# Kernel tuning notes

Hardware: AMD Instinct MI355X
Metric: run time of the kernel (lower is better)

## Reference

```python
import jax, jax.numpy as jnp
import numpy as np

HBLK = 16  # hadamard / nvfp4 block size
FP4_LEVELS = jnp.array([0.0, 0.5, 1.0, 1.5, 2.0, 3.0, 4.0, 6.0], dtype=jnp.float32)
FP4_MIDS = jnp.array([0.25, 0.75, 1.25, 1.75, 2.5, 3.5, 5.0], dtype=jnp.float32)


def _hadamard(n):
    H = np.array([[1.0]])
    while H.shape[0] < n:
        H = np.block([[H, H], [H, -H]])
    return jnp.asarray(H / np.sqrt(n), dtype=jnp.float32)  # orthonormal

H16 = _hadamard(HBLK)


def rht_forward(x, signs):
    # x: [M, K], K % 16 == 0 (no padding needed). Random sign diag then block Hadamard.
    M, K = x.shape
    xb = x.reshape(M, K // HBLK, HBLK)
    return ((xb * signs) @ H16).reshape(M, K)


def q_emulate(x):
    # NVFP4 quantize->dequantize along last dim: blocks of 16, E4M3 block scale = amax/6,
    # round-to-nearest onto E2M1 grid {0,.5,1,1.5,2,3,4,6} (signed).
    M, K = x.shape
    xb = x.reshape(M, K // HBLK, HBLK)
    amax = jnp.max(jnp.abs(xb), axis=-1, keepdims=True)
    scale = (amax / 6.0).astype(jnp.float8_e4m3fn).astype(x.dtype)
    safe = jnp.where(scale == 0, 1.0, scale)
    a = jnp.clip(jnp.abs(xb) / safe, 0.0, 6.0)
    q = FP4_LEVELS[jnp.searchsorted(FP4_MIDS, a)]
    return (jnp.sign(xb) * q * scale).reshape(M, K)


def setup_inputs() -> dict:
    key = jax.random.key(0)
    kx, kw, kb, ks1, ks2 = jax.random.split(key, 5)
    IN, OUT = 4096, 4096
    x = jax.random.normal(kx, (4, 2048, IN), dtype=jnp.float32)
    weight = jax.random.normal(kw, (OUT, IN), dtype=jnp.float32) / np.sqrt(IN)
    bound = 1.0 / np.sqrt(IN)
    bias = jax.random.uniform(kb, (OUT,), dtype=jnp.float32, minval=-bound, maxval=bound)
    signs_in = jnp.where(jax.random.bernoulli(ks1, 0.5, (HBLK,)), 1.0, -1.0).astype(jnp.float32)
    signs_grad = jnp.where(jax.random.bernoulli(ks2, 0.5, (HBLK,)), 1.0, -1.0).astype(jnp.float32)
    return {"x": x, "weight": weight, "bias": bias, "signs_in": signs_in, "signs_grad": signs_grad}


def reference(x, weight, bias, signs_in, signs_grad):
    # signs_grad only used in backward (kept for interface parity).
    x_flat = x.reshape(-1, x.shape[-1])
    x_q = q_emulate(rht_forward(x_flat, signs_in))
    w_q = q_emulate(rht_forward(weight, signs_in))
    y = x_q @ w_q.T + bias
    return y.reshape(*x.shape[:-1], weight.shape[0])
```

## Files before the change

### kernel.cpp

```cpp
#include <hip/hip_runtime.h>
#include <stdint.h>


typedef __bf16 bf16x8 __attribute__((ext_vector_type(8)));
typedef float f32x4 __attribute__((ext_vector_type(4)));


__device__ __forceinline__ float e4m3_rt(float x) {
    unsigned int u = __float_as_uint(x);
    int ex = (int)((u >> 23) & 0xffu) - 127;
    if (ex < -6) ex = -6;
    float qs = __uint_as_float((unsigned)(127 + 3 - ex) << 23);
    float qi = __uint_as_float((unsigned)(127 + ex - 3) << 23);
    return rintf(x * qs) * qi;
}

__global__ __launch_bounds__(256) void quant_rht_kernel(
    const float* __restrict__ X, const float* __restrict__ signs,
    uint16_t* __restrict__ Q, int ngroups)
{
    (void)ngroups;
    __shared__ uint4 sbuf[1024];
    const int t = threadIdx.x;
    const size_t gbase = (size_t)blockIdx.x * 256;

    const uint4* src = (const uint4*)(X + gbase * 16);
#pragma unroll
    for (int it = 0; it < 4; ++it) {
        int c = it * 256 + t;
        sbuf[c ^ ((c >> 3) & 7)] = src[c];
    }
    __syncthreads();

    float tv[16];
#pragma unroll
    for (int i = 0; i < 4; ++i) {
        int c = 4 * t + i;
        uint4 u = sbuf[c ^ ((c >> 3) & 7)];
        tv[4 * i + 0] = __uint_as_float(u.x);
        tv[4 * i + 1] = __uint_as_float(u.y);
        tv[4 * i + 2] = __uint_as_float(u.z);
        tv[4 * i + 3] = __uint_as_float(u.w);
    }

#pragma unroll
    for (int i = 0; i < 16; i++) tv[i] *= signs[i];

#pragma unroll
    for (int len = 1; len < 16; len <<= 1) {
#pragma unroll
        for (int i = 0; i < 16; i += 2 * len) {
#pragma unroll
            for (int j = 0; j < len; j++) {
                float a = tv[i + j], b = tv[i + j + len];
                tv[i + j] = a + b;
                tv[i + j + len] = a - b;
            }
        }
    }
    float amax = 0.0f;
#pragma unroll
    for (int i = 0; i < 16; i++) { tv[i] *= 0.25f; amax = fmaxf(amax, fabsf(tv[i])); }

    float scale = e4m3_rt(amax / 6.0f);
    float safe = (scale == 0.0f) ? 1.0f : scale;

    unsigned int w[8];
#pragma unroll
    for (int i = 0; i < 8; i++) {
        float d01[2];
#pragma unroll
        for (int h = 0; h < 2; h++) {
            float x = tv[2 * i + h];
            float aa = fminf(fabsf(x) / safe, 6.0f);
            float q = aa > 2.5f ? (aa > 5.0f ? 6.0f : (aa > 3.5f ? 4.0f : 3.0f))
                                : (aa > 1.25f ? (aa > 1.75f ? 2.0f : 1.5f)
                                              : (aa > 0.75f ? 1.0f
                                                 : (aa > 0.25f ? 0.5f : 0.0f)));
            d01[h] = copysignf(q * scale, x);
        }
        w[i] = (__float_as_uint(d01[0]) >> 16) |
               (__float_as_uint(d01[1]) & 0xFFFF0000u);
    }

    __syncthreads();
    {
        int c0 = 2 * t, c1 = 2 * t + 1;
        sbuf[c0 ^ ((c0 >> 3) & 7)] = make_uint4(w[0], w[1], w[2], w[3]);
        sbuf[c1 ^ ((c1 >> 3) & 7)] = make_uint4(w[4], w[5], w[6], w[7]);
    }
    __syncthreads();

    uint4* dst = (uint4*)(Q + gbase * 16);
#pragma unroll
    for (int it = 0; it < 2; ++it) {
        int c = it * 256 + t;
        dst[c] = sbuf[c ^ ((c >> 3) & 7)];
    }
}


#define BM 256
#define BN 256

__global__ __launch_bounds__(512, 2) void gemm_bt_bias(
    const uint16_t* __restrict__ A,
    const uint16_t* __restrict__ B,
    const float* __restrict__ bias,
    float* __restrict__ C,
    int M, int N, int K)
{
    __shared__ uint4 sh[8][1024];

    const int tid  = threadIdx.x;
    const int lane = tid & 63;
    const int wave = tid >> 6;
    const int wm = wave >> 2, wn = wave & 3;
    const int lm = lane & 15, g4 = lane >> 4;
    const int bn = blockIdx.x, bm = blockIdx.y;

    const int NT  = K >> 6;
    const int NHT = NT << 2;

    const int p0 = tid, p1 = 512 + tid;
    const int c0 = p0 ^ ((p0 >> 3) & 7);
    const int c1 = p1 ^ ((p1 >> 3) & 7);
    const uint16_t* asrc0 = A + (size_t)(bm * BM + (c0 >> 2)) * K + (c0 & 3) * 8;
    const uint16_t* asrc1 = A + (size_t)(bm * BM + (c1 >> 2)) * K + (c1 & 3) * 8;
    const uint16_t* bsrc0 = B + (size_t)(bn * BN + (c0 >> 2)) * K + (c0 & 3) * 8;
    const uint16_t* bsrc1 = B + (size_t)(bn * BN + (c1 >> 2)) * K + (c1 & 3) * 8;
    char* ldsd0 = (char*)&sh[0][0] + p0 * 16;
    char* ldsd1 = (char*)&sh[0][0] + p1 * 16;

    int aPos[8], bPos[4];
#pragma unroll
    for (int f = 0; f < 8; ++f) {
        int c = (wm * 128 + f * 16 + lm) * 4 + g4;
        aPos[f] = c ^ ((c >> 3) & 7);
    }
#pragma unroll
    for (int f = 0; f < 4; ++f) {
        int c = (wn * 64 + f * 16 + lm) * 4 + g4;
        bPos[f] = c ^ ((c >> 3) & 7);
    }

    f32x4 acc[8][4];
#pragma unroll
    for (int i = 0; i < 8; ++i)
#pragma unroll
        for (int j = 0; j < 4; ++j) acc[i][j] = (f32x4){0.f, 0.f, 0.f, 0.f};
    bf16x8 bfr[4];

#define STAGE(jj) do {                                                        \
    int _j = (jj);                                                            \
    int _koff = (_j < NHT) ? (((_j >> 2) << 6) | (((_j >> 1) & 1) << 5)) : 0; \
    int _sb = (_j & 7) << 14;                                                 \
    const uint16_t* _s0 = (_j & 1) ? bsrc0 : asrc0;                           \
    const uint16_t* _s1 = (_j & 1) ? bsrc1 : asrc1;                           \
    __builtin_amdgcn_global_load_lds(                                         \
        (const __attribute__((address_space(1))) unsigned int*)(_s0 + _koff), \
        (__attribute__((address_space(3))) unsigned int*)(ldsd0 + _sb),       \
        16, 0, 0);                                                            \
    __builtin_amdgcn_global_load_lds(                                         \
        (const __attribute__((address_space(1))) unsigned int*)(_s1 + _koff), \
        (__attribute__((address_space(3))) unsigned int*)(ldsd1 + _sb),       \
        16, 0, 0);                                                            \
} while (0)

#define PHASE(PAR, KS, RH, Q, GATE) do {                                      \
    bf16x8 af_[4];                                                            \
    _Pragma("unroll")                                                         \
    for (int _i = 0; _i < 4; ++_i)                                            \
        af_[_i] = __builtin_bit_cast(bf16x8,                                  \
            sh[4*(PAR) + 2*(KS)][aPos[4*(RH) + _i]]);                         \
    if ((Q) & 1) {                                                            \
        _Pragma("unroll")                                                     \
        for (int _jj = 0; _jj < 4; ++_jj)                                     \
            bfr[_jj] = __builtin_bit_cast(bf16x8,                             \
                sh[4*(PAR) + 2*(KS) + 1][bPos[_jj]]);                         \
    }                                                                         \
    STAGE(hb + 5 + (Q));                                                      \
    __builtin_amdgcn_s_barrier();                                             \
    asm volatile("s_waitcnt lgkmcnt(0)" ::: "memory");                        \
    __builtin_amdgcn_s_setprio(1);                                            \
    _Pragma("unroll")                                                         \
    for (int _i = 0; _i < 4; ++_i)                                            \
        _Pragma("unroll")                                                     \
        for (int _jj = 0; _jj < 4; ++_jj)                                     \
            acc[4*(RH) + _i][_jj] = __builtin_amdgcn_mfma_f32_16x16x32_bf16(  \
                af_[_i], bfr[_jj], acc[4*(RH) + _i][_jj], 0, 0, 0);           \
    __builtin_amdgcn_s_setprio(0);                                            \
    if (GATE) asm volatile("s_waitcnt vmcnt(4)" ::: "memory");                \
    __builtin_amdgcn_s_barrier();                                             \
} while (0)

    STAGE(0); STAGE(1); STAGE(2); STAGE(3); STAGE(4); STAGE(5);
    asm volatile("s_waitcnt vmcnt(4)" ::: "memory");
    __builtin_amdgcn_s_barrier();

    const int NT2 = NT >> 1;
    for (int it2 = 0; it2 < NT2; ++it2) {
        const int hb = it2 << 3;
        PHASE(0, 0, 0, 1, 0);
        PHASE(0, 0, 1, 2, 0);
        PHASE(0, 1, 0, 3, 0);
        PHASE(0, 1, 1, 4, 1);
        PHASE(1, 0, 0, 5, 0);
        PHASE(1, 0, 1, 6, 0);
        PHASE(1, 1, 0, 7, 0);
        PHASE(1, 1, 1, 8, 1);
    }
    asm volatile("s_waitcnt vmcnt(0)" ::: "memory");

#undef PHASE
#undef STAGE

#pragma unroll
    for (int j = 0; j < 4; ++j) {
        int col = bn * BN + wn * 64 + j * 16 + lm;
        float bj = bias[col];
#pragma unroll
        for (int i = 0; i < 8; ++i) {
            int row0 = bm * BM + wm * 128 + i * 16 + g4 * 4;
#pragma unroll
            for (int r = 0; r < 4; ++r) {
                C[(size_t)(row0 + r) * (size_t)N + col] = acc[i][j][r] + bj;
            }
        }
    }
}


extern "C" void kernel_launch(void* const* d_in, const int* in_sizes, int n_in,
                              void* d_out, int out_size, void* d_ws, size_t ws_size,
                              hipStream_t stream)
{
    const float* x        = (const float*)d_in[0];
    const float* w        = (const float*)d_in[1];
    const float* bias     = (const float*)d_in[2];
    const float* signs_in = (const float*)d_in[3];

    const int OUT = in_sizes[2];
    const int IN  = in_sizes[1] / OUT;
    const int M   = in_sizes[0] / IN;

    uint16_t* xq = (uint16_t*)d_ws;
    uint16_t* wq = xq + (size_t)M * (size_t)IN;
    (void)ws_size; (void)n_in; (void)out_size;

    int ngx = (int)((size_t)M * IN / 16);
    int ngw = (int)((size_t)OUT * IN / 16);
    quant_rht_kernel<<<ngx / 256, 256, 0, stream>>>(x, signs_in, xq, ngx);
    quant_rht_kernel<<<ngw / 256, 256, 0, stream>>>(w, signs_in, wq, ngw);

    dim3 grid(OUT / BN, M / BM);
    gemm_bt_bias<<<grid, 512, 0, stream>>>(xq, wq, bias, (float*)d_out, M, OUT, IN);
}
```

Baseline: 495.9 us.

## Double-buffer GEMM LDS fragments and simplify quant kernel to direct vector loads

The GEMM main loop now keeps double-buffered A and B register fragments, loading the next window's fragments from LDS while the current window's MFMAs run. This removes the per-phase lgkmcnt(0) wait and one of the two barriers per phase, and moves the staging distance and vmcnt gating. The quantize kernel drops its LDS transpose and instead has each thread load its 16 floats with float4 loads and store the result directly, trading coalescing through shared memory for fewer barriers. The new schedule's correctness depends on the revised staging offsets and barrier placement being consistent with the LDS buffer reuse.

```diff
diff --git a/kernel.cpp b/kernel.cpp
--- a/kernel.cpp
+++ b/kernel.cpp
@@ -15,88 +15,73 @@
     return rintf(x * qs) * qi;
 }
 
+__device__ __forceinline__ float quant1(float tv, float safe, float scale) {
+    float aa = fminf(fabsf(tv) / safe, 6.0f);
+    float q = aa > 2.5f ? (aa > 5.0f ? 6.0f : (aa > 3.5f ? 4.0f : 3.0f))
+                        : (aa > 1.25f ? (aa > 1.75f ? 2.0f : 1.5f)
+                                      : (aa > 0.75f ? 1.0f
+                                         : (aa > 0.25f ? 0.5f : 0.0f)));
+    return copysignf(q * scale, tv);
+}
+
+__device__ __forceinline__ unsigned pack2(float lo, float hi) {
+    return (__float_as_uint(lo) >> 16) | (__float_as_uint(hi) & 0xFFFF0000u);
+}
+
 __global__ __launch_bounds__(256) void quant_rht_kernel(
     const float* __restrict__ X, const float* __restrict__ signs,
     uint16_t* __restrict__ Q, int ngroups)
 {
-    (void)ngroups;
-    __shared__ uint4 sbuf[1024];
-    const int t = threadIdx.x;
-    const size_t gbase = (size_t)blockIdx.x * 256;
-
-    const uint4* src = (const uint4*)(X + gbase * 16);
-#pragma unroll
-    for (int it = 0; it < 4; ++it) {
-        int c = it * 256 + t;
-        sbuf[c ^ ((c >> 3) & 7)] = src[c];
-    }
-    __syncthreads();
-
-    float tv[16];
-#pragma unroll
-    for (int i = 0; i < 4; ++i) {
-        int c = 4 * t + i;
-        uint4 u = sbuf[c ^ ((c >> 3) & 7)];
-        tv[4 * i + 0] = __uint_as_float(u.x);
-        tv[4 * i + 1] = __uint_as_float(u.y);
-        tv[4 * i + 2] = __uint_as_float(u.z);
-        tv[4 * i + 3] = __uint_as_float(u.w);
-    }
-
-#pragma unroll
-    for (int i = 0; i < 16; i++) tv[i] *= signs[i];
-
-#pragma unroll
-    for (int len = 1; len < 16; len <<= 1) {
-#pragma unroll
-        for (int i = 0; i < 16; i += 2 * len) {
-#pragma unroll
-            for (int j = 0; j < len; j++) {
-                float a = tv[i + j], b = tv[i + j + len];
-                tv[i + j] = a + b;
-                tv[i + j + len] = a - b;
-            }
-        }
-    }
-    float amax = 0.0f;
-#pragma unroll
-    for (int i = 0; i < 16; i++) { tv[i] *= 0.25f; amax = fmaxf(amax, fabsf(tv[i])); }
+    int gid = blockIdx.x * 256 + threadIdx.x;
+    if (gid >= ngroups) return;
+
+    const float4* p = (const float4*)(X + (size_t)gid * 16);
+    float4 v0 = p[0], v1 = p[1], v2 = p[2], v3 = p[3];
+    const float4* sp = (const float4*)signs;
+    float4 s0 = sp[0], s1 = sp[1], s2 = sp[2], s3 = sp[3];
+
+    float t0 = v0.x * s0.x, t1 = v0.y * s0.y, t2 = v0.z * s0.z, t3 = v0.w * s0.w;
+    float t4 = v1.x * s1.x, t5 = v1.y * s1.y, t6 = v1.z * s1.z, t7 = v1.w * s1.w;
+    float t8 = v2.x * s2.x, t9 = v2.y * s2.y, t10 = v2.z * s2.z, t11 = v2.w * s2.w;
+    float t12 = v3.x * s3.x, t13 = v3.y * s3.y, t14 = v3.z * s3.z, t15 = v3.w * s3.w;
+
+#define BT(a, b) { float _s = (a) + (b), _d = (a) - (b); (a) = _s; (b) = _d; }
+    BT(t0,t1)  BT(t2,t3)  BT(t4,t5)   BT(t6,t7)
+    BT(t8,t9)  BT(t10,t11) BT(t12,t13) BT(t14,t15)
+    BT(t0,t2)  BT(t1,t3)  BT(t4,t6)   BT(t5,t7)
+    BT(t8,t10) BT(t9,t11) BT(t12,t14) BT(t13,t15)
+    BT(t0,t4)  BT(t1,t5)  BT(t2,t6)   BT(t3,t7)
+    BT(t8,t12) BT(t9,t13) BT(t10,t14) BT(t11,t15)
+    BT(t0,t8)  BT(t1,t9)  BT(t2,t10)  BT(t3,t11)
+    BT(t4,t12) BT(t5,t13) BT(t6,t14)  BT(t7,t15)
+#undef BT
+
+    t0 *= 0.25f;  t1 *= 0.25f;  t2 *= 0.25f;  t3 *= 0.25f;
+    t4 *= 0.25f;  t5 *= 0.25f;  t6 *= 0.25f;  t7 *= 0.25f;
+    t8 *= 0.25f;  t9 *= 0.25f;  t10 *= 0.25f; t11 *= 0.25f;
+    t12 *= 0.25f; t13 *= 0.25f; t14 *= 0.25f; t15 *= 0.25f;
+
+    float amax = fmaxf(
+        fmaxf(fmaxf(fmaxf(fabsf(t0), fabsf(t1)), fmaxf(fabsf(t2), fabsf(t3))),
+              fmaxf(fmaxf(fabsf(t4), fabsf(t5)), fmaxf(fabsf(t6), fabsf(t7)))),
+        fmaxf(fmaxf(fmaxf(fabsf(t8), fabsf(t9)), fmaxf(fabsf(t10), fabsf(t11))),
+              fmaxf(fmaxf(fabsf(t12), fabsf(t13)), fmaxf(fabsf(t14), fabsf(t15)))));
 
     float scale = e4m3_rt(amax / 6.0f);
     float safe = (scale == 0.0f) ? 1.0f : scale;
 
-    unsigned int w[8];
-#pragma unroll
-    for (int i = 0; i < 8; i++) {
-        float d01[2];
-#pragma unroll
-        for (int h = 0; h < 2; h++) {
-            float x = tv[2 * i + h];
-            float aa = fminf(fabsf(x) / safe, 6.0f);
-            float q = aa > 2.5f ? (aa > 5.0f ? 6.0f : (aa > 3.5f ? 4.0f : 3.0f))
-                                : (aa > 1.25f ? (aa > 1.75f ? 2.0f : 1.5f)
-                                              : (aa > 0.75f ? 1.0f
-                                                 : (aa > 0.25f ? 0.5f : 0.0f)));
-            d01[h] = copysignf(q * scale, x);
-        }
-        w[i] = (__float_as_uint(d01[0]) >> 16) |
-               (__float_as_uint(d01[1]) & 0xFFFF0000u);
-    }
-
-    __syncthreads();
-    {
-        int c0 = 2 * t, c1 = 2 * t + 1;
-        sbuf[c0 ^ ((c0 >> 3) & 7)] = make_uint4(w[0], w[1], w[2], w[3]);
-        sbuf[c1 ^ ((c1 >> 3) & 7)] = make_uint4(w[4], w[5], w[6], w[7]);
-    }
-    __syncthreads();
-
-    uint4* dst = (uint4*)(Q + gbase * 16);
-#pragma unroll
-    for (int it = 0; it < 2; ++it) {
-        int c = it * 256 + t;
-        dst[c] = sbuf[c ^ ((c >> 3) & 7)];
-    }
+    unsigned w0 = pack2(quant1(t0, safe, scale),  quant1(t1, safe, scale));
+    unsigned w1 = pack2(quant1(t2, safe, scale),  quant1(t3, safe, scale));
+    unsigned w2 = pack2(quant1(t4, safe, scale),  quant1(t5, safe, scale));
+    unsigned w3 = pack2(quant1(t6, safe, scale),  quant1(t7, safe, scale));
+    unsigned w4 = pack2(quant1(t8, safe, scale),  quant1(t9, safe, scale));
+    unsigned w5 = pack2(quant1(t10, safe, scale), quant1(t11, safe, scale));
+    unsigned w6 = pack2(quant1(t12, safe, scale), quant1(t13, safe, scale));
+    unsigned w7 = pack2(quant1(t14, safe, scale), quant1(t15, safe, scale));
+
+    uint4* q4 = (uint4*)(Q + (size_t)gid * 16);
+    q4[0] = make_uint4(w0, w1, w2, w3);
+    q4[1] = make_uint4(w4, w5, w6, w7);
 }
 
 
@@ -149,7 +134,8 @@
     for (int i = 0; i < 8; ++i)
 #pragma unroll
         for (int j = 0; j < 4; ++j) acc[i][j] = (f32x4){0.f, 0.f, 0.f, 0.f};
-    bf16x8 bfr[4];
+
+    bf16x8 a0[4], a1[4], b0[4], b1[4];
 
 #define STAGE(jj) do {                                                        \
     int _j = (jj);                                                            \
@@ -167,52 +153,55 @@
         16, 0, 0);                                                            \
 } while (0)
 
-#define PHASE(PAR, KS, RH, Q, GATE) do {                                      \
-    bf16x8 af_[4];                                                            \
+#define WIN(ARH, CA, CB, NA, NSA, NRH, LOADB, NB, NSB, SJ, GATE) do {         \
     _Pragma("unroll")                                                         \
     for (int _i = 0; _i < 4; ++_i)                                            \
-        af_[_i] = __builtin_bit_cast(bf16x8,                                  \
-            sh[4*(PAR) + 2*(KS)][aPos[4*(RH) + _i]]);                         \
-    if ((Q) & 1) {                                                            \
+        NA[_i] = __builtin_bit_cast(bf16x8, sh[NSA][aPos[4*(NRH) + _i]]);     \
+    if (LOADB) {                                                              \
         _Pragma("unroll")                                                     \
         for (int _jj = 0; _jj < 4; ++_jj)                                     \
-            bfr[_jj] = __builtin_bit_cast(bf16x8,                             \
-                sh[4*(PAR) + 2*(KS) + 1][bPos[_jj]]);                         \
+            NB[_jj] = __builtin_bit_cast(bf16x8, sh[NSB][bPos[_jj]]);         \
     }                                                                         \
-    STAGE(hb + 5 + (Q));                                                      \
-    __builtin_amdgcn_s_barrier();                                             \
-    asm volatile("s_waitcnt lgkmcnt(0)" ::: "memory");                        \
+    STAGE(hb + (SJ));                                                         \
+    if (GATE) asm volatile("s_waitcnt vmcnt(4)" ::: "memory");                \
+    __builtin_amdgcn_sched_barrier(0);                                        \
     __builtin_amdgcn_s_setprio(1);                                            \
     _Pragma("unroll")                                                         \
     for (int _i = 0; _i < 4; ++_i)                                            \
         _Pragma("unroll")                                                     \
         for (int _jj = 0; _jj < 4; ++_jj)                                     \
-            acc[4*(RH) + _i][_jj] = __builtin_amdgcn_mfma_f32_16x16x32_bf16(  \
-                af_[_i], bfr[_jj], acc[4*(RH) + _i][_jj], 0, 0, 0);           \
+            acc[4*(ARH) + _i][_jj] = __builtin_amdgcn_mfma_f32_16x16x32_bf16( \
+                CA[_i], CB[_jj], acc[4*(ARH) + _i][_jj], 0, 0, 0);            \
     __builtin_amdgcn_s_setprio(0);                                            \
-    if (GATE) asm volatile("s_waitcnt vmcnt(4)" ::: "memory");                \
+    __builtin_amdgcn_sched_barrier(0);                                        \
     __builtin_amdgcn_s_barrier();                                             \
 } while (0)
 
     STAGE(0); STAGE(1); STAGE(2); STAGE(3); STAGE(4); STAGE(5);
-    asm volatile("s_waitcnt vmcnt(4)" ::: "memory");
+    asm volatile("s_waitcnt vmcnt(8)" ::: "memory");
     __builtin_amdgcn_s_barrier();
+#pragma unroll
+    for (int i = 0; i < 4; ++i)
+        a1[i] = __builtin_bit_cast(bf16x8, sh[0][aPos[i]]);
+#pragma unroll
+    for (int j = 0; j < 4; ++j)
+        b0[j] = __builtin_bit_cast(bf16x8, sh[1][bPos[j]]);
 
     const int NT2 = NT >> 1;
     for (int it2 = 0; it2 < NT2; ++it2) {
         const int hb = it2 << 3;
-        PHASE(0, 0, 0, 1, 0);
-        PHASE(0, 0, 1, 2, 0);
-        PHASE(0, 1, 0, 3, 0);
-        PHASE(0, 1, 1, 4, 1);
-        PHASE(1, 0, 0, 5, 0);
-        PHASE(1, 0, 1, 6, 0);
-        PHASE(1, 1, 0, 7, 0);
-        PHASE(1, 1, 1, 8, 1);
-    }
-    asm volatile("s_waitcnt vmcnt(0)" ::: "memory");
-
-#undef PHASE
+        WIN(0, a1, b0, a0, 0, 1, 0, b1, 0,  6, 1);
+        WIN(1, a0, b0, a1, 2, 0, 1, b1, 3,  7, 0);
+        WIN(0, a1, b1, a0, 2, 1, 0, b0, 0,  8, 1);
+        WIN(1, a0, b1, a1, 4, 0, 1, b0, 5,  9, 0);
+        WIN(0, a1, b0, a0, 4, 1, 0, b1, 0, 10, 1);
+        WIN(1, a0, b0, a1, 6, 0, 1, b1, 7, 11, 0);
+        WIN(0, a1, b1, a0, 6, 1, 0, b0, 0, 12, 1);
+        WIN(1, a0, b1, a1, 0, 0, 1, b0, 1, 13, 0);
+    }
+    asm volatile("s_waitcnt vmcnt(0) lgkmcnt(0)" ::: "memory");
+
+#undef WIN
 #undef STAGE
 
 #pragma unroll
@@ -250,8 +239,8 @@
 
     int ngx = (int)((size_t)M * IN / 16);
     int ngw = (int)((size_t)OUT * IN / 16);
-    quant_rht_kernel<<<ngx / 256, 256, 0, stream>>>(x, signs_in, xq, ngx);
-    quant_rht_kernel<<<ngw / 256, 256, 0, stream>>>(w, signs_in, wq, ngw);
+    quant_rht_kernel<<<(ngx + 255) / 256, 256, 0, stream>>>(x, signs_in, xq, ngx);
+    quant_rht_kernel<<<(ngw + 255) / 256, 256, 0, stream>>>(w, signs_in, wq, ngw);
 
     dim3 grid(OUT / BN, M / BM);
     gemm_bt_bias<<<grid, 512, 0, stream>>>(xq, wq, bias, (float*)d_out, M, OUT, IN);
```

After: 487.7 us. Within noise of the previous version (-1.7%).
